# Kernel tuning notes

Measured on AMD Instinct MI355X. Metric: run time of the kernel, lower is better.

Reference implementation:

```python
import jax, jax.numpy as jnp
import numpy as np

COMMITMENT_COST = 0.25


def setup_inputs() -> dict:
    key = jax.random.key(0)
    k1, k2 = jax.random.split(key)
    B, D, H, W = 64, 64, 32, 32
    K = 512
    x = jax.random.normal(k1, (B, D, H, W), dtype=jnp.float32)
    # torch init: uniform_(-1/K, 1/K)
    codebook = jax.random.uniform(k2, (K, D), dtype=jnp.float32,
                                  minval=-1.0 / K, maxval=1.0 / K)
    return {"x": x, "codebook": codebook}


def reference(x, codebook):
    B, D, H, W = x.shape
    K = codebook.shape[0]
    in_re = jnp.transpose(x, (0, 2, 3, 1))          # [B,H,W,D]
    flat = in_re.reshape(-1, D)                      # [N,D], N=B*H*W
    dist = (jnp.sum(flat * flat, axis=1, keepdims=True)
            + jnp.sum(codebook * codebook, axis=1)
            - 2.0 * jnp.matmul(flat, codebook.T))    # [N,K]
    idx = jnp.argmin(dist, axis=1)                   # [N]
    encoding = jax.nn.one_hot(idx, K, dtype=jnp.float32)  # [N,K]
    softmax_histogram = jnp.sum(jax.nn.softmax(-dist, axis=-1).reshape(B, -1, K), axis=1)  # [B,K]
    quantized = jnp.matmul(encoding, codebook).reshape(in_re.shape)  # [B,H,W,D]
    e_latent_loss = jnp.mean((jax.lax.stop_gradient(quantized) - in_re) ** 2)
    q_latent_loss = jnp.mean((quantized - jax.lax.stop_gradient(in_re)) ** 2)
    loss = q_latent_loss + COMMITMENT_COST * e_latent_loss
    # straight-through estimator
    quant_st = in_re + jax.lax.stop_gradient(quantized - in_re)
    avg_probs = jnp.mean(encoding, axis=0)
    perplexity = jnp.exp(-jnp.sum(avg_probs * jnp.log(avg_probs + 1e-10)))
    quant_out = jnp.transpose(quant_st, (0, 3, 1, 2))  # back to NCHW
    encoding_indice = idx.reshape(B, -1)               # [B, H*W]
    # per-batch histogram of code usage == sum of one-hots over spatial dim
    index_program = jnp.sum(encoding.reshape(B, -1, K), axis=1)  # [B,K]
    return (quant_out, loss, perplexity, encoding_indice, index_program, softmax_histogram)
```

## Files before the change

kernel.cpp:

```cpp
#include <hip/hip_runtime.h>


#define OFF_LOSS 4194304
#define OFF_PERP 4194305
#define OFF_ENC  4194306
#define OFF_IP   4259842
#define OFF_SH   4292610

#define WS_CBT   0
#define WS_CE2   32768
#define WS_SHP   33280
#define WS_LOSS  1081856


typedef float f16v __attribute__((ext_vector_type(16)));

__global__ __launch_bounds__(256) void vq_prep(const float* __restrict__ cb,
                                               float* __restrict__ ws)
{
    const int t  = blockIdx.x * 256 + threadIdx.x;
    const int kg = t >> 4;
    const int j  = t & 15;
    const float4 v = ((const float4*)cb)[(kg << 4) + j];
    float pr = v.x * v.x + v.y * v.y + v.z * v.z + v.w * v.w;
    #pragma unroll
    for (int off = 1; off < 16; off <<= 1) pr += __shfl_xor(pr, off, 16);
    if (j == 0) ws[WS_CE2 + kg] = pr;
    const int kc = kg >> 7, kl = kg & 127;
    float* base = ws + WS_CBT + (kc << 13) + (j << 9) + kl;
    base[0]   = v.x;
    base[128] = v.y;
    base[256] = v.z;
    base[384] = v.w;
}

#define FMA4(ACC, AV, K4) \
    ACC[(K4) + 0] = fmaf((AV), bq.x, ACC[(K4) + 0]); \
    ACC[(K4) + 1] = fmaf((AV), bq.y, ACC[(K4) + 1]); \
    ACC[(K4) + 2] = fmaf((AV), bq.z, ACC[(K4) + 2]); \
    ACC[(K4) + 3] = fmaf((AV), bq.w, ACC[(K4) + 3]);

#define ST_CST() do { \
    float4* c4 = (float4*)csT; \
    c4[t] = pv0; c4[256 + t] = pv1; c4[512 + t] = pv2; c4[768 + t] = pv3; \
    c4[1024 + t] = pv4; c4[1280 + t] = pv5; c4[1536 + t] = pv6; c4[1792 + t] = pv7; \
} while (0)

#define PREFETCH(KC1) do { \
    pv0 = cbT4[((KC1) << 11) + t];        pv1 = cbT4[((KC1) << 11) + 256 + t]; \
    pv2 = cbT4[((KC1) << 11) + 512 + t];  pv3 = cbT4[((KC1) << 11) + 768 + t]; \
    pv4 = cbT4[((KC1) << 11) + 1024 + t]; pv5 = cbT4[((KC1) << 11) + 1280 + t]; \
    pv6 = cbT4[((KC1) << 11) + 1536 + t]; pv7 = cbT4[((KC1) << 11) + 1792 + t]; \
} while (0)

#define GEMM_CHUNK(KC) do { \
    __syncthreads(); \
    ST_CST(); \
    if ((KC) < 3) PREFETCH((KC) + 1); \
    __syncthreads(); \
    _Pragma("unroll 2") \
    for (int db = 0; db < 16; ++db) { \
        const float* cbase = &csT[(db << 9) + (tc << 2)]; \
        _Pragma("unroll") \
        for (int j = 0; j < 4; ++j) { \
            const int d = (db << 2) + j; \
            const float4 a0 = *(const float4*)&xs[(d << 5) + (tr << 2)]; \
            const float4 bq = *(const float4*)&cbase[j << 7]; \
            FMA4(acc0, a0.x, (KC) << 2) \
            FMA4(acc1, a0.y, (KC) << 2) \
            FMA4(acc2, a0.z, (KC) << 2) \
            FMA4(acc3, a0.w, (KC) << 2) \
        } \
    } \
} while (0)

#define EPI_C(C, ACC) { \
    const int k = (((C) >> 2) << 7) + (tc << 2) + ((C) & 3); \
    const float t1 = xxr + ce2[k]; \
    const float dist = t1 - 2.f * ACC[C]; \
    ACC[C] = dist; \
    if (dist < m) { m = dist; bk = k; } }

#define EXP_C(C, ACC) { \
    const float e = __expf(m - ACC[C]); \
    ACC[C] = e; z += e; }

#define ROW_EPI(I, ACC, INVZ) do { \
    const int row = (tr << 2) + (I); \
    const float xxr = sxx[row]; \
    float m = 1e30f; int bk = 0; \
    EPI_C(0, ACC)  EPI_C(1, ACC)  EPI_C(2, ACC)  EPI_C(3, ACC) \
    EPI_C(4, ACC)  EPI_C(5, ACC)  EPI_C(6, ACC)  EPI_C(7, ACC) \
    EPI_C(8, ACC)  EPI_C(9, ACC)  EPI_C(10, ACC) EPI_C(11, ACC) \
    EPI_C(12, ACC) EPI_C(13, ACC) EPI_C(14, ACC) EPI_C(15, ACC) \
    _Pragma("unroll") \
    for (int off = 1; off < 32; off <<= 1) { \
        const float mo = __shfl_xor(m, off, 32); \
        const int   ko = __shfl_xor(bk, off, 32); \
        if (mo < m || (mo == m && ko < bk)) { m = mo; bk = ko; } \
    } \
    float z = 0.f; \
    EXP_C(0, ACC)  EXP_C(1, ACC)  EXP_C(2, ACC)  EXP_C(3, ACC) \
    EXP_C(4, ACC)  EXP_C(5, ACC)  EXP_C(6, ACC)  EXP_C(7, ACC) \
    EXP_C(8, ACC)  EXP_C(9, ACC)  EXP_C(10, ACC) EXP_C(11, ACC) \
    EXP_C(12, ACC) EXP_C(13, ACC) EXP_C(14, ACC) EXP_C(15, ACC) \
    _Pragma("unroll") \
    for (int off = 1; off < 32; off <<= 1) z += __shfl_xor(z, off, 32); \
    INVZ = 1.f / z; \
    if (tc == 0) { \
        sidx[row] = bk; \
        enc[((size_t)b << 10) + row0 + row] = (float)bk; \
    } \
} while (0)

#define HIST_C(C) { \
    const int k = (((C) >> 2) << 7) + (tc << 2) + ((C) & 3); \
    float cs = 0.f; \
    cs += acc0[C] * invz0; cs += acc1[C] * invz1; \
    cs += acc2[C] * invz2; cs += acc3[C] * invz3; \
    atomicAdd(&shist[k], cs); }

__global__ __launch_bounds__(256, 1) void vq_main(
    const float* __restrict__ x, const float* __restrict__ cb,
    const float* __restrict__ wsc,
    float* __restrict__ wso,
    float* __restrict__ out)
{
    __shared__ float  xs[64 * 32];
    __shared__ float  csT[64 * 128];
    __shared__ float  ce2[512];
    __shared__ float  sxx[32];
    __shared__ int    sidx[32];

    const int t    = threadIdx.x;
    const int blk  = blockIdx.x;
    const int b    = blk >> 5;
    const int row0 = (blk & 31) << 5;
    const int tr   = t >> 5;
    const int tc   = t & 31;

    const float4* cbT4 = (const float4*)(wsc + WS_CBT);

    {
        const float4* xb4 = (const float4*)(x + ((size_t)b << 16) + row0);
        #pragma unroll
        for (int p = 0; p < 2; ++p) {
            const int fi = (p << 8) + t;
            const int d  = fi >> 3;
            const int r4 = fi & 7;
            *(float4*)&xs[(d << 5) + (r4 << 2)] = xb4[(d << 8) + r4];
        }
    }
    if (t < 128) ((float4*)ce2)[t] = ((const float4*)(wsc + WS_CE2))[t];

    float4 pv0, pv1, pv2, pv3, pv4, pv5, pv6, pv7;
    PREFETCH(0);

    __syncthreads();
    if (t < 32) {
        float s = 0.f;
        for (int d = 0; d < 64; ++d) { const float v = xs[(d << 5) + t]; s = fmaf(v, v, s); }
        sxx[t] = s;
    }

    f16v acc0 = 0.f, acc1 = 0.f, acc2 = 0.f, acc3 = 0.f;

    GEMM_CHUNK(0);
    GEMM_CHUNK(1);
    GEMM_CHUNK(2);
    GEMM_CHUNK(3);

    float* enc = out + OFF_ENC;
    float invz0, invz1, invz2, invz3;
    ROW_EPI(0, acc0, invz0);
    ROW_EPI(1, acc1, invz1);
    ROW_EPI(2, acc2, invz2);
    ROW_EPI(3, acc3, invz3);

    __syncthreads();

    float* shist = csT;
    shist[t] = 0.f; shist[t + 256] = 0.f;
    __syncthreads();
    HIST_C(0)  HIST_C(1)  HIST_C(2)  HIST_C(3)
    HIST_C(4)  HIST_C(5)  HIST_C(6)  HIST_C(7)
    HIST_C(8)  HIST_C(9)  HIST_C(10) HIST_C(11)
    HIST_C(12) HIST_C(13) HIST_C(14) HIST_C(15)
    __syncthreads();
    {
        float* wsh = wso + WS_SHP + ((size_t)blk << 9);
        wsh[t]       = shist[t];
        wsh[t + 256] = shist[t + 256];
    }

    const int r4 = (t & 7) << 2;
    const int dq = t >> 3;
    const int c0 = sidx[r4], c1 = sidx[r4 + 1], c2 = sidx[r4 + 2], c3 = sidx[r4 + 3];
    float lsum = 0.f;
    #pragma unroll
    for (int p = 0; p < 2; ++p) {
        const int d = (p << 5) + dq;
        float4 q;
        q.x = cb[(c0 << 6) + d];
        q.y = cb[(c1 << 6) + d];
        q.z = cb[(c2 << 6) + d];
        q.w = cb[(c3 << 6) + d];
        const float4 xv = *(const float4*)&xs[(d << 5) + r4];
        const float d0 = q.x - xv.x, d1 = q.y - xv.y, d2 = q.z - xv.z, d3 = q.w - xv.w;
        lsum = fmaf(d0, d0, lsum); lsum = fmaf(d1, d1, lsum);
        lsum = fmaf(d2, d2, lsum); lsum = fmaf(d3, d3, lsum);
        *(float4*)&out[(((size_t)(b << 6) + d) << 10) + row0 + r4] = q;
    }
    #pragma unroll
    for (int off = 1; off < 64; off <<= 1) lsum += __shfl_xor(lsum, off, 64);
    if ((t & 63) == 0) wso[WS_LOSS + (blk << 2) + (t >> 6)] = lsum;
}

__global__ __launch_bounds__(512) void vq_reduce(const float* __restrict__ ws,
                                                 float* __restrict__ out)
{
    __shared__ int hist[512];
    const int b = blockIdx.x, t = threadIdx.x;
    const float* p = ws + WS_SHP + ((size_t)b << 14) + t;
    float s = 0.f;
    #pragma unroll
    for (int j = 0; j < 32; ++j) s += p[j << 9];
    out[OFF_SH + (b << 9) + t] = s;
    hist[t] = 0;
    __syncthreads();
    const float* enc = out + OFF_ENC + ((size_t)b << 10);
    const int ca = (int)enc[t];
    const int cbn = (int)enc[t + 512];
    atomicAdd(&hist[ca], 1);
    atomicAdd(&hist[cbn], 1);
    __syncthreads();
    out[OFF_IP + (b << 9) + t] = (float)hist[t];
}

__global__ __launch_bounds__(512) void vq_final(const float* __restrict__ ws,
                                                float* __restrict__ out)
{
    __shared__ float red[8], red2[8];
    const int t = threadIdx.x;
    const float* ip = out + OFF_IP;
    float c0 = 0.f, c1 = 0.f, c2 = 0.f, c3 = 0.f;
    #pragma unroll
    for (int bb = 0; bb < 64; bb += 4) {
        c0 += ip[((bb + 0) << 9) + t];
        c1 += ip[((bb + 1) << 9) + t];
        c2 += ip[((bb + 2) << 9) + t];
        c3 += ip[((bb + 3) << 9) + t];
    }
    const float c = (c0 + c1) + (c2 + c3);
    const float pav = c * (1.0f / 65536.f);
    float h = pav * logf(pav + 1e-10f);
    const float* wl = ws + WS_LOSS;
    float ls = 0.f;
    #pragma unroll
    for (int j = 0; j < 16; ++j) ls += wl[(j << 9) + t];
    #pragma unroll
    for (int off = 1; off < 64; off <<= 1) {
        h  += __shfl_xor(h, off, 64);
        ls += __shfl_xor(ls, off, 64);
    }
    if ((t & 63) == 0) { red[t >> 6] = h; red2[t >> 6] = ls; }
    __syncthreads();
    if (t == 0) {
        float H = 0.f, L = 0.f;
        #pragma unroll
        for (int w = 0; w < 8; ++w) { H += red[w]; L += red2[w]; }
        out[OFF_PERP] = expf(-H);
        out[OFF_LOSS] = L * (1.25f / 4194304.f);
    }
}

extern "C" void kernel_launch(void* const* d_in, const int* in_sizes, int n_in,
                              void* d_out, int out_size, void* d_ws, size_t ws_size,
                              hipStream_t stream)
{
    const float* x  = (const float*)d_in[0];
    const float* cb = (const float*)d_in[1];
    float* out = (float*)d_out;
    float* ws  = (float*)d_ws;
    (void)ws_size;

    vq_prep  <<<32,   256, 0, stream>>>(cb, ws);
    vq_main  <<<2048, 256, 0, stream>>>(x, cb, ws, ws, out);
    vq_reduce<<<64,   512, 0, stream>>>(ws, out);
    vq_final <<<1,    512, 0, stream>>>(ws, out);
}
```

Baseline: 190.5 us.

## Use direct global-to-LDS loads and merge reduce/final kernels via last-block counter

Codebook and input tiles are now staged into shared memory with global_load_lds builtins instead of going through registers, which removes the register prefetch buffers. In exchange, the previous overlap between prefetching the next chunk and computing the current one is lost: each stage is now load, sync, compute. The reduce and final kernels are fused into one tail kernel, where the last block, found through an atomic counter, computes perplexity and loss. This saves one kernel launch but adds threadfences and an atomic.

```diff
diff --git a/kernel.cpp b/kernel.cpp
--- a/kernel.cpp
+++ b/kernel.cpp
@@ -11,13 +11,22 @@
 #define WS_CE2   32768
 #define WS_SHP   33280
 #define WS_LOSS  1081856
+#define WS_CNT   1090048
 
 
 typedef float f16v __attribute__((ext_vector_type(16)));
+
+typedef __attribute__((address_space(1))) const void g_void;
+typedef __attribute__((address_space(3))) void lds_void;
+#define GLOAD_LDS(G, S) \
+    __builtin_amdgcn_global_load_lds((g_void*)(G), (lds_void*)(S), 16, 0, 0)
 
 __global__ __launch_bounds__(256) void vq_prep(const float* __restrict__ cb,
                                                float* __restrict__ ws)
 {
+    if (blockIdx.x == 0 && threadIdx.x == 0)
+        ((int*)ws)[WS_CNT] = 0;
+
     const int t  = blockIdx.x * 256 + threadIdx.x;
     const int kg = t >> 4;
     const int j  = t & 15;
@@ -40,24 +49,18 @@
     ACC[(K4) + 2] = fmaf((AV), bq.z, ACC[(K4) + 2]); \
     ACC[(K4) + 3] = fmaf((AV), bq.w, ACC[(K4) + 3]);
 
-#define ST_CST() do { \
-    float4* c4 = (float4*)csT; \
-    c4[t] = pv0; c4[256 + t] = pv1; c4[512 + t] = pv2; c4[768 + t] = pv3; \
-    c4[1024 + t] = pv4; c4[1280 + t] = pv5; c4[1536 + t] = pv6; c4[1792 + t] = pv7; \
+#define STAGE_CST(KC) do { \
+    GLOAD_LDS(&cbT4[((KC) << 11) + t],        &csT4[t]); \
+    GLOAD_LDS(&cbT4[((KC) << 11) + 256 + t],  &csT4[256 + t]); \
+    GLOAD_LDS(&cbT4[((KC) << 11) + 512 + t],  &csT4[512 + t]); \
+    GLOAD_LDS(&cbT4[((KC) << 11) + 768 + t],  &csT4[768 + t]); \
+    GLOAD_LDS(&cbT4[((KC) << 11) + 1024 + t], &csT4[1024 + t]); \
+    GLOAD_LDS(&cbT4[((KC) << 11) + 1280 + t], &csT4[1280 + t]); \
+    GLOAD_LDS(&cbT4[((KC) << 11) + 1536 + t], &csT4[1536 + t]); \
+    GLOAD_LDS(&cbT4[((KC) << 11) + 1792 + t], &csT4[1792 + t]); \
 } while (0)
 
-#define PREFETCH(KC1) do { \
-    pv0 = cbT4[((KC1) << 11) + t];        pv1 = cbT4[((KC1) << 11) + 256 + t]; \
-    pv2 = cbT4[((KC1) << 11) + 512 + t];  pv3 = cbT4[((KC1) << 11) + 768 + t]; \
-    pv4 = cbT4[((KC1) << 11) + 1024 + t]; pv5 = cbT4[((KC1) << 11) + 1280 + t]; \
-    pv6 = cbT4[((KC1) << 11) + 1536 + t]; pv7 = cbT4[((KC1) << 11) + 1792 + t]; \
-} while (0)
-
-#define GEMM_CHUNK(KC) do { \
-    __syncthreads(); \
-    ST_CST(); \
-    if ((KC) < 3) PREFETCH((KC) + 1); \
-    __syncthreads(); \
+#define GEMM_COMPUTE(KC) do { \
     _Pragma("unroll 2") \
     for (int db = 0; db < 16; ++db) { \
         const float* cbase = &csT[(db << 9) + (tc << 2)]; \
@@ -140,6 +143,7 @@
     const int tc   = t & 31;
 
     const float4* cbT4 = (const float4*)(wsc + WS_CBT);
+    float4* csT4 = (float4*)csT;
 
     {
         const float4* xb4 = (const float4*)(x + ((size_t)b << 16) + row0);
@@ -148,15 +152,14 @@
             const int fi = (p << 8) + t;
             const int d  = fi >> 3;
             const int r4 = fi & 7;
-            *(float4*)&xs[(d << 5) + (r4 << 2)] = xb4[(d << 8) + r4];
+            GLOAD_LDS(&xb4[(d << 8) + r4], &xs[(d << 5) + (r4 << 2)]);
         }
     }
+    STAGE_CST(0);
     if (t < 128) ((float4*)ce2)[t] = ((const float4*)(wsc + WS_CE2))[t];
 
-    float4 pv0, pv1, pv2, pv3, pv4, pv5, pv6, pv7;
-    PREFETCH(0);
-
-    __syncthreads();
+    __syncthreads();
+
     if (t < 32) {
         float s = 0.f;
         for (int d = 0; d < 64; ++d) { const float v = xs[(d << 5) + t]; s = fmaf(v, v, s); }
@@ -165,10 +168,19 @@
 
     f16v acc0 = 0.f, acc1 = 0.f, acc2 = 0.f, acc3 = 0.f;
 
-    GEMM_CHUNK(0);
-    GEMM_CHUNK(1);
-    GEMM_CHUNK(2);
-    GEMM_CHUNK(3);
+    GEMM_COMPUTE(0);
+    __syncthreads();
+    STAGE_CST(1);
+    __syncthreads();
+    GEMM_COMPUTE(1);
+    __syncthreads();
+    STAGE_CST(2);
+    __syncthreads();
+    GEMM_COMPUTE(2);
+    __syncthreads();
+    STAGE_CST(3);
+    __syncthreads();
+    GEMM_COMPUTE(3);
 
     float* enc = out + OFF_ENC;
     float invz0, invz1, invz2, invz3;
@@ -216,10 +228,11 @@
     if ((t & 63) == 0) wso[WS_LOSS + (blk << 2) + (t >> 6)] = lsum;
 }
 
-__global__ __launch_bounds__(512) void vq_reduce(const float* __restrict__ ws,
-                                                 float* __restrict__ out)
+__global__ __launch_bounds__(512) void vq_tail(float* __restrict__ ws,
+                                               float* __restrict__ out)
 {
     __shared__ int hist[512];
+    __shared__ int s_last;
     const int b = blockIdx.x, t = threadIdx.x;
     const float* p = ws + WS_SHP + ((size_t)b << 14) + t;
     float s = 0.f;
@@ -229,19 +242,20 @@
     hist[t] = 0;
     __syncthreads();
     const float* enc = out + OFF_ENC + ((size_t)b << 10);
-    const int ca = (int)enc[t];
+    const int ca  = (int)enc[t];
     const int cbn = (int)enc[t + 512];
     atomicAdd(&hist[ca], 1);
     atomicAdd(&hist[cbn], 1);
     __syncthreads();
     out[OFF_IP + (b << 9) + t] = (float)hist[t];
-}
-
-__global__ __launch_bounds__(512) void vq_final(const float* __restrict__ ws,
-                                                float* __restrict__ out)
-{
+
+    __threadfence();
+    if (t == 0) s_last = (atomicAdd(&((int*)ws)[WS_CNT], 1) == 63);
+    __syncthreads();
+    if (!s_last) return;
+    __threadfence();
+
     __shared__ float red[8], red2[8];
-    const int t = threadIdx.x;
     const float* ip = out + OFF_IP;
     float c0 = 0.f, c1 = 0.f, c2 = 0.f, c3 = 0.f;
     #pragma unroll
@@ -284,8 +298,7 @@
     float* ws  = (float*)d_ws;
     (void)ws_size;
 
-    vq_prep  <<<32,   256, 0, stream>>>(cb, ws);
-    vq_main  <<<2048, 256, 0, stream>>>(x, cb, ws, ws, out);
-    vq_reduce<<<64,   512, 0, stream>>>(ws, out);
-    vq_final <<<1,    512, 0, stream>>>(ws, out);
+    vq_prep <<<32,   256, 0, stream>>>(cb, ws);
+    vq_main <<<2048, 256, 0, stream>>>(x, cb, ws, ws, out);
+    vq_tail <<<64,   512, 0, stream>>>(ws, out);
 }
```

Result: no change. 192.4 us (+1.0%).
